# Kernel tuning notes

Measured on AMD Instinct MI355X. Metric: run time of the kernel, lower is better.

Reference implementation:

```python
import jax, jax.numpy as jnp
import numpy as np

N = 512          # Cartesian grid size (nRead)
C = 16           # n_coils
K = 262144       # n non-uniform k-space samples (~512 spokes x 512 readouts)


def setup_inputs() -> dict:
    key = jax.random.key(0)
    ks = jax.random.split(key, 6)
    x_real = jax.random.normal(ks[0], (C, K), jnp.float32)
    x_imag = jax.random.normal(ks[1], (C, K), jnp.float32)
    csm_real = jax.random.normal(ks[2], (C, N, N), jnp.float32)
    csm_imag = jax.random.normal(ks[3], (C, N, N), jnp.float32)
    # normalized k-space coordinates in [-0.5, 0.5)
    traj = jax.random.uniform(ks[4], (K, 2), jnp.float32, -0.5, 0.5)
    # density compensation weights (positive)
    dcf = jax.random.uniform(ks[5], (K,), jnp.float32)
    return dict(x_real=x_real, x_imag=x_imag, csm_real=csm_real,
                csm_imag=csm_imag, traj=traj, dcf=dcf)


def reference(x_real, x_imag, csm_real, csm_imag, traj, dcf):
    # Adjoint gridding NUFFT with density compensation + coil-sensitivity combine.
    # 1) density-compensate the multicoil non-Cartesian samples
    x = (x_real + 1j * x_imag) * dcf                      # [C, K] complex64
    # 2) grid (scatter-add) onto the Cartesian k-space grid (nearest-cell gridding)
    t = jax.lax.stop_gradient(traj)
    idx = jnp.round((t + 0.5) * N).astype(jnp.int32) % N  # [K, 2]
    iy, ix = idx[:, 0], idx[:, 1]
    grid = jnp.zeros((C, N, N), jnp.complex64).at[:, iy, ix].add(x)
    # 3) centered inverse FFT to image space (adjoint of DFT, scaled by N^2)
    img = jnp.fft.fftshift(
        jnp.fft.ifft2(jnp.fft.ifftshift(grid, axes=(-2, -1)), axes=(-2, -1)),
        axes=(-2, -1)) * (N * N)                          # [C, N, N]
    # 4) coil combine with conjugate sensitivity maps
    csm = csm_real + 1j * csm_imag
    out = jnp.sum(jnp.conj(csm) * img, axis=0)            # [N, N] complex64
    # return real/imag stacked, with batch dim (mimics numpy2tensor add_batch_dim)
    return jnp.stack([out.real, out.imag])[None]          # [1, 2, N, N]
```

## Files before the change

### kernel.cpp

```cpp
#include <hip/hip_runtime.h>
#include <math.h>

#define N 512
#define NN (N * N)
#define C 16
#define K 262144
#define LOG2N 9

#define SK(e) ((e) + ((e) >> 4))
#define LROW 544

__device__ __forceinline__ void rad4(float4* stripe, int p0, int h,
                                     float c1, float s1, float c2, float s2) {
    float4 x0 = stripe[SK(p0)];
    float4 x1 = stripe[SK(p0 + h)];
    float4 x2 = stripe[SK(p0 + 2 * h)];
    float4 x3 = stripe[SK(p0 + 3 * h)];
    float4 t, e0, e1, e2, e3, u, v;
    t.x = c1 * x1.x - s1 * x1.y;  t.y = c1 * x1.y + s1 * x1.x;
    t.z = c1 * x1.z - s1 * x1.w;  t.w = c1 * x1.w + s1 * x1.z;
    e0 = make_float4(x0.x + t.x, x0.y + t.y, x0.z + t.z, x0.w + t.w);
    e1 = make_float4(x0.x - t.x, x0.y - t.y, x0.z - t.z, x0.w - t.w);
    t.x = c1 * x3.x - s1 * x3.y;  t.y = c1 * x3.y + s1 * x3.x;
    t.z = c1 * x3.z - s1 * x3.w;  t.w = c1 * x3.w + s1 * x3.z;
    e2 = make_float4(x2.x + t.x, x2.y + t.y, x2.z + t.z, x2.w + t.w);
    e3 = make_float4(x2.x - t.x, x2.y - t.y, x2.z - t.z, x2.w - t.w);
    u.x = c2 * e2.x - s2 * e2.y;  u.y = c2 * e2.y + s2 * e2.x;
    u.z = c2 * e2.z - s2 * e2.w;  u.w = c2 * e2.w + s2 * e2.z;
    stripe[SK(p0)]         = make_float4(e0.x + u.x, e0.y + u.y, e0.z + u.z, e0.w + u.w);
    stripe[SK(p0 + 2 * h)] = make_float4(e0.x - u.x, e0.y - u.y, e0.z - u.z, e0.w - u.w);
    v.x = -s2 * e3.x - c2 * e3.y;  v.y = c2 * e3.x - s2 * e3.y;
    v.z = -s2 * e3.z - c2 * e3.w;  v.w = c2 * e3.z - s2 * e3.w;
    stripe[SK(p0 + h)]     = make_float4(e1.x + v.x, e1.y + v.y, e1.z + v.z, e1.w + v.w);
    stripe[SK(p0 + 3 * h)] = make_float4(e1.x - v.x, e1.y - v.y, e1.z - v.z, e1.w - v.w);
}

__device__ __forceinline__ void fft512_wave(float4* stripe, int l) {
#pragma unroll
    for (int i = 0; i < 2; ++i) {
        int g = l + (i << 6);
        rad4(stripe, g * 4, 1, 1.f, 0.f, 1.f, 0.f);
    }
    asm volatile("s_waitcnt lgkmcnt(0)" ::: "memory");
#pragma unroll
    for (int fs = 1; fs < 4; ++fs) {
        int h = 1 << (2 * fs);
#pragma unroll
        for (int i = 0; i < 2; ++i) {
            int g = l + (i << 6);
            int j = g & (h - 1);
            int grp = g >> (2 * fs);
            int p0 = (grp << (2 * fs + 2)) + j;
            float a1 = 6.283185307179586f * (float)j / (float)(2 * h);
            float a2 = 0.5f * a1;
            float s1, c1, s2, c2;
            __sincosf(a1, &s1, &c1);
            __sincosf(a2, &s2, &c2);
            rad4(stripe, p0, h, c1, s1, c2, s2);
        }
        asm volatile("s_waitcnt lgkmcnt(0)" ::: "memory");
    }
#pragma unroll
    for (int i = 0; i < 4; ++i) {
        int b2 = l + (i << 6);
        float ang = 6.283185307179586f * (float)b2 * (1.0f / 512.0f);
        float sn, cs;
        __sincosf(ang, &sn, &cs);
        float4 v = stripe[SK(b2 + 256)];
        float4 u = stripe[SK(b2)];
        float tr0 = cs * v.x - sn * v.y;
        float ti0 = cs * v.y + sn * v.x;
        float tr1 = cs * v.z - sn * v.w;
        float ti1 = cs * v.w + sn * v.z;
        stripe[SK(b2 + 256)] = make_float4(u.x - tr0, u.y - ti0, u.z - tr1, u.w - ti1);
        stripe[SK(b2)]       = make_float4(u.x + tr0, u.y + ti0, u.z + tr1, u.w + ti1);
    }
    asm volatile("s_waitcnt lgkmcnt(0)" ::: "memory");
}


__global__ __launch_bounds__(256) void prep_hist_kernel(const float2* __restrict__ traj,
                                                        const float* __restrict__ dcf,
                                                        float2* __restrict__ cw,
                                                        int* __restrict__ count) {
    int k = blockIdx.x * 256 + threadIdx.x;
    float2 t = traj[k];
    int iy = __float2int_rn((t.x + 0.5f) * (float)N) & (N - 1);
    int ix = __float2int_rn((t.y + 0.5f) * (float)N) & (N - 1);
    int cl = iy * N + ix;
    float s = ((iy + ix) & 1) ? -1.0f : 1.0f;
    cw[k] = make_float2(__int_as_float(cl), dcf[k] * s);
    atomicAdd(&count[cl], 1);
}

__global__ __launch_bounds__(256) void scan_reduce_kernel(const int* __restrict__ count,
                                                          int* __restrict__ bsum) {
    __shared__ int sd[256];
    int t = threadIdx.x;
    const int4* c4 = (const int4*)count;
    int4 v = c4[blockIdx.x * 256 + t];
    sd[t] = v.x + v.y + v.z + v.w;
    __syncthreads();
    for (int d = 128; d > 0; d >>= 1) {
        if (t < d) sd[t] += sd[t + d];
        __syncthreads();
    }
    if (t == 0) bsum[blockIdx.x] = sd[0];
}

__global__ __launch_bounds__(256) void scan_final2_kernel(const int* __restrict__ count,
                                                          const int* __restrict__ bsum,
                                                          int* __restrict__ offs,
                                                          int* __restrict__ cursor) {
    __shared__ int sb[256];
    __shared__ int sd[256];
    int t = threadIdx.x;
    int b = blockIdx.x;
    int vb = bsum[t];
    sb[t] = vb;
    __syncthreads();
    for (int d = 1; d < 256; d <<= 1) {
        int tmp = (t >= d) ? sb[t - d] : 0;
        __syncthreads();
        sb[t] += tmp;
        __syncthreads();
    }
    int4 c4 = ((const int4*)count)[b * 256 + t];
    int s = c4.x + c4.y + c4.z + c4.w;
    sd[t] = s;
    __syncthreads();
    for (int d = 1; d < 256; d <<= 1) {
        int tmp = (t >= d) ? sd[t - d] : 0;
        __syncthreads();
        sd[t] += tmp;
        __syncthreads();
    }
    int bexc = sb[b] - bsum[b];
    int base = bexc + sd[t] - s;
    int4 o;
    o.x = base;
    o.y = base + c4.x;
    o.z = base + c4.x + c4.y;
    o.w = base + c4.x + c4.y + c4.z;
    ((int4*)offs)[b * 256 + t] = o;
    ((int4*)cursor)[b * 256 + t] = o;
    if (b == 0 && t == 0) offs[NN] = K;
}

__global__ __launch_bounds__(256) void payload_kernel(const float* __restrict__ xr,
                                                      const float* __restrict__ xi,
                                                      const float2* __restrict__ cw,
                                                      int* __restrict__ cursor,
                                                      float2* __restrict__ pay) {
    __shared__ float tR[256][17];
    __shared__ float tI[256][17];
    __shared__ int   sp[256];
    __shared__ float sw[256];
    int t = threadIdx.x;
    int k0 = blockIdx.x * 256;
#pragma unroll
    for (int c = 0; c < C; ++c) {
        tR[t][c] = xr[(size_t)c * K + k0 + t];
        tI[t][c] = xi[(size_t)c * K + k0 + t];
    }
    float2 cwv = cw[k0 + t];
    int cl = __float_as_int(cwv.x);
    sp[t] = atomicAdd(&cursor[cl], 1);
    sw[t] = cwv.y;
    __syncthreads();
    int sg = t >> 4, l = t & 15;
    for (int j = sg; j < 256; j += 16) {
        int pp = sp[j];
        float ww = sw[j];
        pay[(size_t)pp * 16 + l] = make_float2(tR[j][l] * ww, tI[j][l] * ww);
    }
}

__global__ __launch_bounds__(256) void build8_kernel(const int* __restrict__ offs,
                                                     const float4* __restrict__ pay4,
                                                     float2* __restrict__ grid) {
    __shared__ float4 lds[4][LROW];
    int bid = blockIdx.x;
    int h = bid & 1;
    int r = bid >> 1;
    int t = threadIdx.x;
    int w = t >> 6;
    int l = t & 63;
    int q = h * 4 + w;
    const int* ro = offs + r * N;

    int sv[8], ev[8];
#pragma unroll
    for (int it = 0; it < 8; ++it) {
        int col = l + (it << 6);
        sv[it] = ro[col];
        ev[it] = ro[col + 1];
    }
    float4 vv[8], vv2[8];
#pragma unroll
    for (int it = 0; it < 8; ++it) {
        vv[it] = make_float4(0.f, 0.f, 0.f, 0.f);
        if (sv[it] < ev[it]) vv[it] = pay4[(size_t)sv[it] * 8 + q];
    }
#pragma unroll
    for (int it = 0; it < 8; ++it) {
        vv2[it] = make_float4(0.f, 0.f, 0.f, 0.f);
        if (sv[it] + 1 < ev[it]) vv2[it] = pay4[(size_t)(sv[it] + 1) * 8 + q];
    }
#pragma unroll
    for (int it = 0; it < 8; ++it) {
        float4 acc = make_float4(vv[it].x + vv2[it].x, vv[it].y + vv2[it].y,
                                 vv[it].z + vv2[it].z, vv[it].w + vv2[it].w);
        for (int p = sv[it] + 2; p < ev[it]; ++p) {
            float4 v2 = pay4[(size_t)p * 8 + q];
            acc.x += v2.x; acc.y += v2.y; acc.z += v2.z; acc.w += v2.w;
        }
        int col = l + (it << 6);
        int bc = (int)(__brev((unsigned)col) >> (32 - LOG2N));
        lds[w][SK(bc)] = acc;
    }
    asm volatile("s_waitcnt lgkmcnt(0)" ::: "memory");

    fft512_wave(&lds[w][0], l);

    int c0 = q * 2;
    float2* g0 = grid + (size_t)c0 * NN + (size_t)r * N;
    float2* g1 = grid + (size_t)(c0 + 1) * NN + (size_t)r * N;
    for (int i = l; i < N; i += 64) {
        float4 v = lds[w][SK(i)];
        g0[i] = make_float2(v.x, v.y);
        g1[i] = make_float2(v.z, v.w);
    }
}

__global__ __launch_bounds__(256) void colfft_kernel(float2* __restrict__ grid) {
    __shared__ float4 lds[4][LROW];
    int blk = blockIdx.x;
    int c = blk >> 6;
    int cg = blk & 63;
    int t = threadIdx.x;
    int w = t >> 6;
    int l = t & 63;
    int colb = cg * 8 + w * 2;
    float2* gp = grid + (size_t)c * NN + colb;

#pragma unroll
    for (int j = 0; j < 8; ++j) {
        int row = l + (j << 6);
        float4 v = *(const float4*)(gp + (size_t)row * N);
        int br = (int)(__brev((unsigned)row) >> (32 - LOG2N));
        lds[w][SK(br)] = v;
    }
    asm volatile("s_waitcnt lgkmcnt(0)" ::: "memory");

    fft512_wave(&lds[w][0], l);

#pragma unroll
    for (int j = 0; j < 8; ++j) {
        int i = l + (j << 6);
        *(float4*)(gp + (size_t)i * N) = lds[w][SK(i)];
    }
}

__global__ __launch_bounds__(256) void combine_kernel(const float* __restrict__ csr,
                                                      const float* __restrict__ csi,
                                                      const float2* __restrict__ grid,
                                                      float* __restrict__ out) {
    int pix = blockIdx.x * 256 + threadIdx.x;
    int ny = pix >> LOG2N, nx = pix & (N - 1);
    float ar = 0.f, ai = 0.f;
#pragma unroll
    for (int c = 0; c < C; ++c) {
        float2 uv = grid[(size_t)c * NN + pix];
        float a = csr[c * NN + pix];
        float b = csi[c * NN + pix];
        ar += a * uv.x + b * uv.y;
        ai += a * uv.y - b * uv.x;
    }
    float s = ((ny + nx) & 1) ? -1.f : 1.f;
    out[pix] = s * ar;
    out[NN + pix] = s * ai;
}

extern "C" void kernel_launch(void* const* d_in, const int* in_sizes, int n_in,
                              void* d_out, int out_size, void* d_ws, size_t ws_size,
                              hipStream_t stream) {
    const float* x_real   = (const float*)d_in[0];
    const float* x_imag   = (const float*)d_in[1];
    const float* csm_real = (const float*)d_in[2];
    const float* csm_imag = (const float*)d_in[3];
    const float2* traj    = (const float2*)d_in[4];
    const float* dcf      = (const float*)d_in[5];
    float* out = (float*)d_out;

    char* ws = (char*)d_ws;
    size_t o = 0;
    float* grid  = (float*)(ws + o); o += (size_t)C * NN * 2 * sizeof(float);
    float2* cw   = (float2*)(ws + o); o += (size_t)K * sizeof(float2);
    int*   count = (int*)(ws + o);   o += (size_t)NN * sizeof(int);
    int*   offs  = (int*)(ws + o);   o += ((size_t)NN + 4) * sizeof(int);
    int*   cursor= (int*)(ws + o);   o += (size_t)NN * sizeof(int);
    float2* pay  = (float2*)(ws + o); o += (size_t)K * 16 * sizeof(float2);
    int*   bsum  = (int*)(ws + o);   o += 256 * sizeof(int);

    (void)hipMemsetAsync(count, 0, (size_t)NN * sizeof(int), stream);

    prep_hist_kernel<<<K / 256, 256, 0, stream>>>(traj, dcf, cw, count);
    scan_reduce_kernel<<<256, 256, 0, stream>>>(count, bsum);
    scan_final2_kernel<<<256, 256, 0, stream>>>(count, bsum, offs, cursor);
    payload_kernel<<<K / 256, 256, 0, stream>>>(x_real, x_imag, cw, cursor, pay);
    build8_kernel<<<N * 2, 256, 0, stream>>>(offs, (const float4*)pay, (float2*)grid);
    colfft_kernel<<<C * 64, 256, 0, stream>>>((float2*)grid);
    combine_kernel<<<NN / 256, 256, 0, stream>>>(csm_real, csm_imag, (float2*)grid, out);
}
```

Before: 200.0 us.

## Use radix-8 FFT stages, drop cw buffer, vectorize histogram and combine

Replaces the radix-4 plus radix-2 512-point FFT with three radix-8 passes, which cuts the number of LDS round trips and barriers. Removes the intermediate cw buffer: the histogram kernel now only counts, and the payload kernel recomputes the cell index and signed weight from traj and dcf. The histogram and combine kernels each process two elements per thread with wider vector loads and stores. The trade-off is more register pressure in rad8 and duplicated index arithmetic.

Result: no change. 200.3 us (+0.1%).

```diff
diff --git a/kernel.cpp b/kernel.cpp
--- a/kernel.cpp
+++ b/kernel.cpp
@@ -10,87 +10,79 @@
 #define SK(e) ((e) + ((e) >> 4))
 #define LROW 544
 
-__device__ __forceinline__ void rad4(float4* stripe, int p0, int h,
-                                     float c1, float s1, float c2, float s2) {
+__device__ __forceinline__ float4 f4add(float4 a, float4 b) {
+    return make_float4(a.x + b.x, a.y + b.y, a.z + b.z, a.w + b.w);
+}
+__device__ __forceinline__ float4 f4sub(float4 a, float4 b) {
+    return make_float4(a.x - b.x, a.y - b.y, a.z - b.z, a.w - b.w);
+}
+__device__ __forceinline__ float4 cmulf4(float4 a, float c, float s) {
+    return make_float4(c * a.x - s * a.y, c * a.y + s * a.x,
+                       c * a.z - s * a.w, c * a.w + s * a.z);
+}
+__device__ __forceinline__ float4 cmuli(float4 a) {
+    return make_float4(-a.y, a.x, -a.w, a.z);
+}
+
+__device__ __forceinline__ void rad8(float4* stripe, int p0, int h, float th1) {
+    float s1, c1, s2, c2, s3, c3;
+    __sincosf(th1, &s1, &c1);
+    __sincosf(0.5f * th1, &s2, &c2);
+    __sincosf(0.25f * th1, &s3, &c3);
+    const float r2 = 0.70710678118654752f;
+    float c3r = r2 * (c3 - s3), s3r = r2 * (c3 + s3);
     float4 x0 = stripe[SK(p0)];
     float4 x1 = stripe[SK(p0 + h)];
     float4 x2 = stripe[SK(p0 + 2 * h)];
     float4 x3 = stripe[SK(p0 + 3 * h)];
-    float4 t, e0, e1, e2, e3, u, v;
-    t.x = c1 * x1.x - s1 * x1.y;  t.y = c1 * x1.y + s1 * x1.x;
-    t.z = c1 * x1.z - s1 * x1.w;  t.w = c1 * x1.w + s1 * x1.z;
-    e0 = make_float4(x0.x + t.x, x0.y + t.y, x0.z + t.z, x0.w + t.w);
-    e1 = make_float4(x0.x - t.x, x0.y - t.y, x0.z - t.z, x0.w - t.w);
-    t.x = c1 * x3.x - s1 * x3.y;  t.y = c1 * x3.y + s1 * x3.x;
-    t.z = c1 * x3.z - s1 * x3.w;  t.w = c1 * x3.w + s1 * x3.z;
-    e2 = make_float4(x2.x + t.x, x2.y + t.y, x2.z + t.z, x2.w + t.w);
-    e3 = make_float4(x2.x - t.x, x2.y - t.y, x2.z - t.z, x2.w - t.w);
-    u.x = c2 * e2.x - s2 * e2.y;  u.y = c2 * e2.y + s2 * e2.x;
-    u.z = c2 * e2.z - s2 * e2.w;  u.w = c2 * e2.w + s2 * e2.z;
-    stripe[SK(p0)]         = make_float4(e0.x + u.x, e0.y + u.y, e0.z + u.z, e0.w + u.w);
-    stripe[SK(p0 + 2 * h)] = make_float4(e0.x - u.x, e0.y - u.y, e0.z - u.z, e0.w - u.w);
-    v.x = -s2 * e3.x - c2 * e3.y;  v.y = c2 * e3.x - s2 * e3.y;
-    v.z = -s2 * e3.z - c2 * e3.w;  v.w = c2 * e3.z - s2 * e3.w;
-    stripe[SK(p0 + h)]     = make_float4(e1.x + v.x, e1.y + v.y, e1.z + v.z, e1.w + v.w);
-    stripe[SK(p0 + 3 * h)] = make_float4(e1.x - v.x, e1.y - v.y, e1.z - v.z, e1.w - v.w);
+    float4 x4 = stripe[SK(p0 + 4 * h)];
+    float4 x5 = stripe[SK(p0 + 5 * h)];
+    float4 x6 = stripe[SK(p0 + 6 * h)];
+    float4 x7 = stripe[SK(p0 + 7 * h)];
+    float4 t;
+    t = cmulf4(x1, c1, s1); float4 y0 = f4add(x0, t), y1 = f4sub(x0, t);
+    t = cmulf4(x3, c1, s1); float4 y2 = f4add(x2, t), y3 = f4sub(x2, t);
+    t = cmulf4(x5, c1, s1); float4 y4 = f4add(x4, t), y5 = f4sub(x4, t);
+    t = cmulf4(x7, c1, s1); float4 y6 = f4add(x6, t), y7 = f4sub(x6, t);
+    t = cmulf4(y2, c2, s2);        float4 z0 = f4add(y0, t), z2 = f4sub(y0, t);
+    t = cmuli(cmulf4(y3, c2, s2)); float4 z1 = f4add(y1, t), z3 = f4sub(y1, t);
+    t = cmulf4(y6, c2, s2);        float4 z4 = f4add(y4, t), z6 = f4sub(y4, t);
+    t = cmuli(cmulf4(y7, c2, s2)); float4 z5 = f4add(y5, t), z7 = f4sub(y5, t);
+    float4 w0 = cmulf4(z4, c3, s3);
+    float4 w1 = cmulf4(z5, c3r, s3r);
+    float4 w2 = cmuli(cmulf4(z6, c3, s3));
+    float4 w3 = cmuli(cmulf4(z7, c3r, s3r));
+    stripe[SK(p0)]         = f4add(z0, w0);
+    stripe[SK(p0 + 4 * h)] = f4sub(z0, w0);
+    stripe[SK(p0 + h)]     = f4add(z1, w1);
+    stripe[SK(p0 + 5 * h)] = f4sub(z1, w1);
+    stripe[SK(p0 + 2 * h)] = f4add(z2, w2);
+    stripe[SK(p0 + 6 * h)] = f4sub(z2, w2);
+    stripe[SK(p0 + 3 * h)] = f4add(z3, w3);
+    stripe[SK(p0 + 7 * h)] = f4sub(z3, w3);
 }
 
 __device__ __forceinline__ void fft512_wave(float4* stripe, int l) {
-#pragma unroll
-    for (int i = 0; i < 2; ++i) {
-        int g = l + (i << 6);
-        rad4(stripe, g * 4, 1, 1.f, 0.f, 1.f, 0.f);
-    }
-    asm volatile("s_waitcnt lgkmcnt(0)" ::: "memory");
-#pragma unroll
-    for (int fs = 1; fs < 4; ++fs) {
-        int h = 1 << (2 * fs);
-#pragma unroll
-        for (int i = 0; i < 2; ++i) {
-            int g = l + (i << 6);
-            int j = g & (h - 1);
-            int grp = g >> (2 * fs);
-            int p0 = (grp << (2 * fs + 2)) + j;
-            float a1 = 6.283185307179586f * (float)j / (float)(2 * h);
-            float a2 = 0.5f * a1;
-            float s1, c1, s2, c2;
-            __sincosf(a1, &s1, &c1);
-            __sincosf(a2, &s2, &c2);
-            rad4(stripe, p0, h, c1, s1, c2, s2);
-        }
-        asm volatile("s_waitcnt lgkmcnt(0)" ::: "memory");
-    }
-#pragma unroll
-    for (int i = 0; i < 4; ++i) {
-        int b2 = l + (i << 6);
-        float ang = 6.283185307179586f * (float)b2 * (1.0f / 512.0f);
-        float sn, cs;
-        __sincosf(ang, &sn, &cs);
-        float4 v = stripe[SK(b2 + 256)];
-        float4 u = stripe[SK(b2)];
-        float tr0 = cs * v.x - sn * v.y;
-        float ti0 = cs * v.y + sn * v.x;
-        float tr1 = cs * v.z - sn * v.w;
-        float ti1 = cs * v.w + sn * v.z;
-        stripe[SK(b2 + 256)] = make_float4(u.x - tr0, u.y - ti0, u.z - tr1, u.w - ti1);
-        stripe[SK(b2)]       = make_float4(u.x + tr0, u.y + ti0, u.z + tr1, u.w + ti1);
-    }
-    asm volatile("s_waitcnt lgkmcnt(0)" ::: "memory");
-}
-
-
-__global__ __launch_bounds__(256) void prep_hist_kernel(const float2* __restrict__ traj,
-                                                        const float* __restrict__ dcf,
-                                                        float2* __restrict__ cw,
+    rad8(stripe, l * 8, 1, 0.0f);
+    asm volatile("s_waitcnt lgkmcnt(0)" ::: "memory");
+    rad8(stripe, (l >> 3) * 64 + (l & 7), 8,
+         6.283185307179586f * (float)(l & 7) * (1.0f / 16.0f));
+    asm volatile("s_waitcnt lgkmcnt(0)" ::: "memory");
+    rad8(stripe, l, 64,
+         6.283185307179586f * (float)l * (1.0f / 128.0f));
+    asm volatile("s_waitcnt lgkmcnt(0)" ::: "memory");
+}
+
+__global__ __launch_bounds__(256) void prep_hist_kernel(const float4* __restrict__ traj2,
                                                         int* __restrict__ count) {
-    int k = blockIdx.x * 256 + threadIdx.x;
-    float2 t = traj[k];
-    int iy = __float2int_rn((t.x + 0.5f) * (float)N) & (N - 1);
-    int ix = __float2int_rn((t.y + 0.5f) * (float)N) & (N - 1);
-    int cl = iy * N + ix;
-    float s = ((iy + ix) & 1) ? -1.0f : 1.0f;
-    cw[k] = make_float2(__int_as_float(cl), dcf[k] * s);
-    atomicAdd(&count[cl], 1);
+    int k2 = blockIdx.x * 256 + threadIdx.x;
+    float4 t2 = traj2[k2];
+    int iy0 = __float2int_rn((t2.x + 0.5f) * (float)N) & (N - 1);
+    int ix0 = __float2int_rn((t2.y + 0.5f) * (float)N) & (N - 1);
+    int iy1 = __float2int_rn((t2.z + 0.5f) * (float)N) & (N - 1);
+    int ix1 = __float2int_rn((t2.w + 0.5f) * (float)N) & (N - 1);
+    atomicAdd(&count[iy0 * N + ix0], 1);
+    atomicAdd(&count[iy1 * N + ix1], 1);
 }
 
 __global__ __launch_bounds__(256) void scan_reduce_kernel(const int* __restrict__ count,
@@ -149,7 +141,8 @@
 
 __global__ __launch_bounds__(256) void payload_kernel(const float* __restrict__ xr,
                                                       const float* __restrict__ xi,
-                                                      const float2* __restrict__ cw,
+                                                      const float2* __restrict__ traj,
+                                                      const float* __restrict__ dcf,
                                                       int* __restrict__ cursor,
                                                       float2* __restrict__ pay) {
     __shared__ float tR[256][17];
@@ -163,10 +156,12 @@
         tR[t][c] = xr[(size_t)c * K + k0 + t];
         tI[t][c] = xi[(size_t)c * K + k0 + t];
     }
-    float2 cwv = cw[k0 + t];
-    int cl = __float_as_int(cwv.x);
+    float2 tr = traj[k0 + t];
+    int iy = __float2int_rn((tr.x + 0.5f) * (float)N) & (N - 1);
+    int ix = __float2int_rn((tr.y + 0.5f) * (float)N) & (N - 1);
+    int cl = iy * N + ix;
     sp[t] = atomicAdd(&cursor[cl], 1);
-    sw[t] = cwv.y;
+    sw[t] = dcf[k0 + t] * (((iy + ix) & 1) ? -1.0f : 1.0f);
     __syncthreads();
     int sg = t >> 4, l = t & 15;
     for (int j = sg; j < 256; j += 16) {
@@ -266,20 +261,24 @@
                                                       const float* __restrict__ csi,
                                                       const float2* __restrict__ grid,
                                                       float* __restrict__ out) {
-    int pix = blockIdx.x * 256 + threadIdx.x;
+    int p2 = blockIdx.x * 256 + threadIdx.x;
+    int pix = p2 * 2;
     int ny = pix >> LOG2N, nx = pix & (N - 1);
-    float ar = 0.f, ai = 0.f;
+    float ar0 = 0.f, ai0 = 0.f, ar1 = 0.f, ai1 = 0.f;
 #pragma unroll
     for (int c = 0; c < C; ++c) {
-        float2 uv = grid[(size_t)c * NN + pix];
-        float a = csr[c * NN + pix];
-        float b = csi[c * NN + pix];
-        ar += a * uv.x + b * uv.y;
-        ai += a * uv.y - b * uv.x;
-    }
-    float s = ((ny + nx) & 1) ? -1.f : 1.f;
-    out[pix] = s * ar;
-    out[NN + pix] = s * ai;
+        float4 uv = ((const float4*)(grid + (size_t)c * NN))[p2];
+        float2 a = ((const float2*)(csr + (size_t)c * NN))[p2];
+        float2 b = ((const float2*)(csi + (size_t)c * NN))[p2];
+        ar0 += a.x * uv.x + b.x * uv.y;
+        ai0 += a.x * uv.y - b.x * uv.x;
+        ar1 += a.y * uv.z + b.y * uv.w;
+        ai1 += a.y * uv.w - b.y * uv.z;
+    }
+    float s0 = ((ny + nx) & 1) ? -1.f : 1.f;
+    float s1 = -s0;
+    ((float2*)out)[p2] = make_float2(s0 * ar0, s1 * ar1);
+    ((float2*)(out + NN))[p2] = make_float2(s0 * ai0, s1 * ai1);
 }
 
 extern "C" void kernel_launch(void* const* d_in, const int* in_sizes, int n_in,
@@ -296,7 +295,6 @@
     char* ws = (char*)d_ws;
     size_t o = 0;
     float* grid  = (float*)(ws + o); o += (size_t)C * NN * 2 * sizeof(float);
-    float2* cw   = (float2*)(ws + o); o += (size_t)K * sizeof(float2);
     int*   count = (int*)(ws + o);   o += (size_t)NN * sizeof(int);
     int*   offs  = (int*)(ws + o);   o += ((size_t)NN + 4) * sizeof(int);
     int*   cursor= (int*)(ws + o);   o += (size_t)NN * sizeof(int);
@@ -305,11 +303,11 @@
 
     (void)hipMemsetAsync(count, 0, (size_t)NN * sizeof(int), stream);
 
-    prep_hist_kernel<<<K / 256, 256, 0, stream>>>(traj, dcf, cw, count);
+    prep_hist_kernel<<<K / 512, 256, 0, stream>>>((const float4*)traj, count);
     scan_reduce_kernel<<<256, 256, 0, stream>>>(count, bsum);
     scan_final2_kernel<<<256, 256, 0, stream>>>(count, bsum, offs, cursor);
-    payload_kernel<<<K / 256, 256, 0, stream>>>(x_real, x_imag, cw, cursor, pay);
+    payload_kernel<<<K / 256, 256, 0, stream>>>(x_real, x_imag, traj, dcf, cursor, pay);
     build8_kernel<<<N * 2, 256, 0, stream>>>(offs, (const float4*)pay, (float2*)grid);
     colfft_kernel<<<C * 64, 256, 0, stream>>>((float2*)grid);
-    combine_kernel<<<NN / 256, 256, 0, stream>>>(csm_real, csm_imag, (float2*)grid, out);
-}
+    combine_kernel<<<NN / 512, 256, 0, stream>>>(csm_real, csm_imag, (float2*)grid, out);
+}
```
